# Kernel tuning notes

Hardware: AMD Instinct MI355X
Metric: run time of the kernel (lower is better)

Reference implementation:

```python
import jax, jax.numpy as jnp
import numpy as np

B, T, D = 8, 1024, 768
H, DH = 12, 64
E, K, DFF = 16, 2, 3072
EPS = 1e-5


def _ln(x, w, b):
    m = x.mean(-1, keepdims=True)
    v = ((x - m) ** 2).mean(-1, keepdims=True)
    return (x - m) * jax.lax.rsqrt(v + EPS) * w + b


def setup_inputs() -> dict:
    key = jax.random.key(0)
    ks = jax.random.split(key, 12)
    s = 0.02
    return {
        "x": jax.random.normal(ks[0], (B, T, D), jnp.float32),
        "ln1_w": jnp.ones((D,), jnp.float32),
        "ln1_b": jnp.zeros((D,), jnp.float32),
        "qkv_w": jax.random.normal(ks[1], (D, 3 * D), jnp.float32) * s,
        "qkv_b": jnp.zeros((3 * D,), jnp.float32),
        "proj_w": jax.random.normal(ks[2], (D, D), jnp.float32) * s,
        "proj_b": jnp.zeros((D,), jnp.float32),
        "ln2_w": jnp.ones((D,), jnp.float32),
        "ln2_b": jnp.zeros((D,), jnp.float32),
        "router_w": jax.random.normal(ks[3], (D, E), jnp.float32) * s,
        "w1": jax.random.normal(ks[4], (E, D, DFF), jnp.float32) * s,
        "b1": jnp.zeros((E, DFF), jnp.float32),
        "w2": jax.random.normal(ks[5], (E, DFF, D), jnp.float32) * s,
        "b2": jnp.zeros((E, D), jnp.float32),
    }


def _block(x, ln1_w, ln1_b, qkv_w, qkv_b, proj_w, proj_b,
           ln2_w, ln2_b, router_w, w1, b1, w2, b2):
    # --- attention ---
    h = _ln(x, ln1_w, ln1_b)
    qkv = h @ qkv_w + qkv_b                      # [B,T,3D]
    q, k, v = jnp.split(qkv, 3, axis=-1)
    q = q.reshape(B, T, H, DH).transpose(0, 2, 1, 3)
    k = k.reshape(B, T, H, DH).transpose(0, 2, 1, 3)
    v = v.reshape(B, T, H, DH).transpose(0, 2, 1, 3)
    scores = jnp.einsum("bhqd,bhkd->bhqk", q, k) / np.sqrt(DH)
    causal = jnp.tril(jnp.ones((T, T), bool))
    scores = jnp.where(causal, scores, -jnp.inf)
    attn = jax.nn.softmax(scores, axis=-1)
    y = jnp.einsum("bhqk,bhkd->bhqd", attn, v)
    y = y.transpose(0, 2, 1, 3).reshape(B, T, D)
    x = x + y @ proj_w + proj_b                  # residual 1

    # --- MoE FFN (dense all-experts, gated combine) ---
    z = _ln(x, ln2_w, ln2_b)                     # [B,T,D]
    probs = jax.nn.softmax(z @ router_w, axis=-1)  # [B,T,E]
    top_p, ix = jax.lax.top_k(probs, K)
    gate = (jax.nn.one_hot(ix, E, dtype=probs.dtype) * top_p[..., None]).sum(-2)  # [B,T,E]
    gate_e = jnp.moveaxis(gate, -1, 0)           # [E,B,T]

    def body(acc, ew):
        g, W1, B1, W2, B2 = ew
        out = jax.nn.gelu(z @ W1 + B1, approximate=False) @ W2 + B2
        return acc + g[..., None] * out, None

    yff, _ = jax.lax.scan(body, jnp.zeros_like(z), (gate_e, w1, b1, w2, b2))
    # MoELayer returns z + yff; Block adds x again (faithful double residual)
    return x + z + yff


def reference(x, ln1_w, ln1_b, qkv_w, qkv_b, proj_w, proj_b,
              ln2_w, ln2_b, router_w, w1, b1, w2, b2):
    return _block(x, ln1_w, ln1_b, qkv_w, qkv_b, proj_w, proj_b,
                  ln2_w, ln2_b, router_w, w1, b1, w2, b2)
```

## Files before the change

### kernel.cpp

```cpp
#include <hip/hip_runtime.h>
#include <math.h>

#define D_MODEL 768
#define T_SEQ   1024
#define B_BATCH 8
#define NTOK    8192
#define H_HEADS 12
#define DHEAD   64
#define NEXP    16
#define DFF     3072
#define NPAIR   16384
#define MAXT128 144
#define MAXT256 80

typedef unsigned short u16;
typedef unsigned int   u32;

typedef __attribute__((ext_vector_type(8))) short bf16x8;
typedef __attribute__((ext_vector_type(4))) float f32x4;
typedef __attribute__((ext_vector_type(4))) u32   u32x4;

__device__ __forceinline__ float bf2f(u16 u) { return __uint_as_float(((u32)u) << 16); }
__device__ __forceinline__ u16 f2bf(float f) {
    u32 u = __float_as_uint(f);
    return (u16)((u + 0x7FFFu + ((u >> 16) & 1u)) >> 16);
}

__device__ __forceinline__ float fast_gelu(float v) {
    float u2 = -1.5957691216f * v * (1.0f + 0.044715f * v * v);
    return v / (1.0f + __expf(u2));
}

__device__ __forceinline__ void gload16(const void* g, void* l) {
    __builtin_amdgcn_global_load_lds((const __attribute__((address_space(1))) void*)g,
                                     (__attribute__((address_space(3))) void*)l, 16, 0, 0);
}

__global__ __launch_bounds__(256) void ln_kernel(const float* __restrict__ x,
                                                 const float* __restrict__ w,
                                                 const float* __restrict__ b,
                                                 u16* __restrict__ out_bf,
                                                 float* __restrict__ out_f) {
    const int row = blockIdx.x;
    const int tid = threadIdx.x;
    const float* xr = x + (size_t)row * D_MODEL;
    float v0 = xr[tid], v1 = xr[tid + 256], v2 = xr[tid + 512];
    float s = v0 + v1 + v2;
    float s2 = v0 * v0 + v1 * v1 + v2 * v2;
#pragma unroll
    for (int o = 32; o > 0; o >>= 1) { s += __shfl_down(s, o); s2 += __shfl_down(s2, o); }
    __shared__ float red[8];
    __shared__ float stats[2];
    const int wid = tid >> 6;
    if ((tid & 63) == 0) { red[wid] = s; red[4 + wid] = s2; }
    __syncthreads();
    if (tid == 0) {
        float ts = red[0] + red[1] + red[2] + red[3];
        float ts2 = red[4] + red[5] + red[6] + red[7];
        float mean = ts * (1.0f / D_MODEL);
        float var = ts2 * (1.0f / D_MODEL) - mean * mean;
        stats[0] = mean;
        stats[1] = rsqrtf(var + 1e-5f);
    }
    __syncthreads();
    const float mean = stats[0], rstd = stats[1];
    u16* orow = out_bf + (size_t)row * D_MODEL;
    float r0 = (v0 - mean) * rstd * w[tid]       + b[tid];
    float r1 = (v1 - mean) * rstd * w[tid + 256] + b[tid + 256];
    float r2 = (v2 - mean) * rstd * w[tid + 512] + b[tid + 512];
    orow[tid] = f2bf(r0); orow[tid + 256] = f2bf(r1); orow[tid + 512] = f2bf(r2);
    if (out_f) {
        float* frow = out_f + (size_t)row * D_MODEL;
        frow[tid] = r0; frow[tid + 256] = r1; frow[tid + 512] = r2;
    }
}

__global__ __launch_bounds__(256) void transpose_cvt(const float* __restrict__ src,
                                                     u16* __restrict__ dst,
                                                     int R, int C) {
    const size_t plane = (size_t)R * C;
    src += (size_t)blockIdx.z * plane;
    dst += (size_t)blockIdx.z * plane;
    __shared__ __align__(16) u16 tile[64][72];
    const int t = threadIdx.x;
    const int r0 = blockIdx.y * 64, c0 = blockIdx.x * 64;
    {
        const int lr = t >> 2, lc = (t & 3) * 16;
        const float* sp = src + (size_t)(r0 + lr) * C + c0 + lc;
        u16 tmp[16];
#pragma unroll
        for (int j = 0; j < 4; ++j) {
            f32x4 f = *(const f32x4*)(sp + j * 4);
            tmp[j * 4 + 0] = f2bf(f[0]); tmp[j * 4 + 1] = f2bf(f[1]);
            tmp[j * 4 + 2] = f2bf(f[2]); tmp[j * 4 + 3] = f2bf(f[3]);
        }
        *(u32x4*)&tile[lr][lc]     = *(const u32x4*)&tmp[0];
        *(u32x4*)&tile[lr][lc + 8] = *(const u32x4*)&tmp[8];
    }
    __syncthreads();
    {
        const int ln = t >> 2, lk0 = (t & 3) * 16;
        u16 o[16];
#pragma unroll
        for (int j = 0; j < 16; ++j) o[j] = tile[lk0 + j][ln];
        u16* d = dst + (size_t)(c0 + ln) * R + r0 + lk0;
        *(u32x4*)&d[0] = *(const u32x4*)&o[0];
        *(u32x4*)&d[8] = *(const u32x4*)&o[8];
    }
}

template <int MODE>
__global__ __launch_bounds__(512, 2) void gemm2ph(
    const u16* __restrict__ A, const u16* __restrict__ Bt,
    const float* __restrict__ bias, void* __restrict__ Cout,
    const int* __restrict__ bucket_tok, const int* __restrict__ offsets,
    const int* __restrict__ counts, const int* __restrict__ desc_e,
    const int* __restrict__ desc_r, const int* __restrict__ tile_cnt,
    int K, int N)
{
    const u32 nwg  = gridDim.x * gridDim.y;
    const u32 orig = blockIdx.x + gridDim.x * blockIdx.y;
    const u32 flat = (nwg & 7u) ? orig : ((orig & 7u) * (nwg >> 3) + (orig >> 3));
    const int bx = (int)(flat % gridDim.x);
    const int by = (int)(flat / gridDim.x);

    int e = 0, r0 = 0, off = 0, ne = 0, row0 = 0;
    const int col0 = bx * 256;
    if constexpr (MODE >= 2) {
        if (by >= *tile_cnt) return;
        e = desc_e[by];
        r0 = desc_r[by];
        off = offsets[e];
        ne = counts[e];
    } else {
        row0 = by * 256;
    }
    if constexpr (MODE == 2) Bt += (size_t)e * D_MODEL * DFF;
    if constexpr (MODE == 3) Bt += (size_t)e * DFF * D_MODEL;

    __shared__ __align__(16) u16 As[2][256 * 64];
    __shared__ __align__(16) u16 Bs[2][256 * 64];

    const int tid = threadIdx.x;
    const int lane = tid & 63;
    const int w = tid >> 6;
    const int wm = w >> 2, wn = w & 3;
    const int fr = lane & 15, fg = lane >> 4;

    const int koff = ((((tid & 7) * 16) ^ (((tid >> 3) & 7) << 4)) >> 1);

    u32 aoff[4], boff[4];
#pragma unroll
    for (int i = 0; i < 4; ++i) {
        const int r = i * 64 + (tid >> 3);
        u32 row;
        if constexpr (MODE == 2) {
            int rb = r0 + r;
            row = (u32)bucket_tok[off + (rb < ne ? rb : 0)];
        } else if constexpr (MODE == 3) {
            int rb = r0 + r;
            row = (u32)(off + (rb < ne ? rb : (ne - 1)));
        } else {
            row = (u32)(row0 + r);
        }
        aoff[i] = row * (u32)K + (u32)koff;
        boff[i] = (u32)(col0 + r) * (u32)K + (u32)koff;
    }

    f32x4 acc[8][4] = {};
    const int nt = K >> 6;

#pragma unroll
    for (int i = 0; i < 4; ++i) gload16(A + aoff[i],  &As[0][(i * 512 + w * 64) * 8]);
#pragma unroll
    for (int i = 0; i < 4; ++i) gload16(Bt + boff[i], &Bs[0][(i * 512 + w * 64) * 8]);
    __syncthreads();

    int cur = 0;
    for (int t = 0; t < nt; ++t) {
        if (t + 1 < nt) {
            const int k0n = (t + 1) * 64;
            const int nxt = cur ^ 1;
#pragma unroll
            for (int i = 0; i < 4; ++i) gload16(A + aoff[i] + k0n,  &As[nxt][(i * 512 + w * 64) * 8]);
#pragma unroll
            for (int i = 0; i < 4; ++i) gload16(Bt + boff[i] + k0n, &Bs[nxt][(i * 512 + w * 64) * 8]);
        }
#pragma unroll
        for (int kk = 0; kk < 2; ++kk) {
            const int sw = ((kk * 64 + fg * 16) ^ ((fr & 7) << 4)) >> 1;
            bf16x8 a[8], b[4];
#pragma unroll
            for (int mi = 0; mi < 8; ++mi)
                a[mi] = *(const bf16x8*)&As[cur][(wm * 128 + mi * 16 + fr) * 64 + sw];
#pragma unroll
            for (int ni = 0; ni < 4; ++ni)
                b[ni] = *(const bf16x8*)&Bs[cur][(wn * 64 + ni * 16 + fr) * 64 + sw];
#pragma unroll
            for (int mi = 0; mi < 8; ++mi)
#pragma unroll
                for (int ni = 0; ni < 4; ++ni)
                    acc[mi][ni] = __builtin_amdgcn_mfma_f32_16x16x32_bf16(a[mi], b[ni], acc[mi][ni], 0, 0, 0);
        }
        if (t + 1 < nt) {
            __syncthreads();
            cur ^= 1;
        }
    }

    __syncthreads();
    float* slab = (float*)&As[0][0] + w * 1088;
    const int er = lane >> 2;
    const int ec = (lane & 3) * 16;
    const int colb = col0 + wn * 64 + ec;

#pragma unroll
    for (int mi = 0; mi < 8; ++mi) {
#pragma unroll
        for (int ni = 0; ni < 4; ++ni)
#pragma unroll
            for (int i = 0; i < 4; ++i)
                slab[(fg * 4 + i) * 68 + ni * 16 + fr] = acc[mi][ni][i];
        __syncthreads();
        f32x4 v[4];
#pragma unroll
        for (int q = 0; q < 4; ++q) v[q] = *(const f32x4*)&slab[er * 68 + ec + q * 4];
        const int lrow = wm * 128 + mi * 16 + er;

        if constexpr (MODE == 0) {
            u16 o[16];
#pragma unroll
            for (int q = 0; q < 4; ++q) {
                f32x4 b4 = *(const f32x4*)&bias[colb + q * 4];
#pragma unroll
                for (int j = 0; j < 4; ++j) o[q * 4 + j] = f2bf(v[q][j] + b4[j]);
            }
            u16* cp = (u16*)Cout + (size_t)(row0 + lrow) * N + colb;
            *(u32x4*)cp       = *(const u32x4*)&o[0];
            *(u32x4*)(cp + 8) = *(const u32x4*)&o[8];
        } else if constexpr (MODE == 2) {
            const int rb = r0 + lrow;
            if (rb < ne) {
                u16 o[16];
#pragma unroll
                for (int q = 0; q < 4; ++q) {
                    f32x4 b4 = *(const f32x4*)&bias[(size_t)e * DFF + colb + q * 4];
#pragma unroll
                    for (int j = 0; j < 4; ++j) o[q * 4 + j] = f2bf(fast_gelu(v[q][j] + b4[j]));
                }
                u16* cp = (u16*)Cout + (size_t)(off + rb) * N + colb;
                *(u32x4*)cp       = *(const u32x4*)&o[0];
                *(u32x4*)(cp + 8) = *(const u32x4*)&o[8];
            }
        } else {
            const int rb = r0 + lrow;
            if (rb < ne) {
                float* cp = (float*)Cout + (size_t)(off + rb) * N + colb;
#pragma unroll
                for (int q = 0; q < 4; ++q) {
                    f32x4 b4 = *(const f32x4*)&bias[(size_t)e * D_MODEL + colb + q * 4];
                    f32x4 o4;
#pragma unroll
                    for (int j = 0; j < 4; ++j) o4[j] = v[q][j] + b4[j];
                    *(f32x4*)(cp + q * 4) = o4;
                }
            }
        }
        if (mi < 7) __syncthreads();
    }
}

template <int MODE>
__global__ __launch_bounds__(512, 4) void gemm256(
    const u16* __restrict__ A, const u16* __restrict__ Bt,
    const float* __restrict__ bias, void* __restrict__ Cout,
    const float* __restrict__ resid,
    int K, int N)
{
    const u32 nwg  = gridDim.x * gridDim.y;
    const u32 orig = blockIdx.x + gridDim.x * blockIdx.y;
    const u32 flat = (nwg & 7u) ? orig : ((orig & 7u) * (nwg >> 3) + (orig >> 3));
    const int bx = (int)(flat % gridDim.x);
    const int by = (int)(flat / gridDim.x);

    const int col0 = bx * 128;
    const int row0 = by * 256;

    __shared__ __align__(16) u16 AsBs[256 * 64 + 128 * 64];
    u16* As = AsBs;
    u16* Bs = AsBs + 256 * 64;

    const int tid = threadIdx.x;
    const int lane = tid & 63;
    const int w = tid >> 6;
    const int wm = w >> 1, wn = w & 1;
    const int fr = lane & 15, fg = lane >> 4;

    const int koff = ((((tid & 7) * 16) ^ (((tid >> 3) & 7) << 4)) >> 1);

    u32 aoff[4];
#pragma unroll
    for (int i = 0; i < 4; ++i)
        aoff[i] = (u32)(row0 + i * 64 + (tid >> 3)) * (u32)K + (u32)koff;
    u32 boff[2];
#pragma unroll
    for (int i = 0; i < 2; ++i)
        boff[i] = (u32)(col0 + i * 64 + (tid >> 3)) * (u32)K + (u32)koff;

    f32x4 acc[4][4] = {};

    for (int k0 = 0; k0 < K; k0 += 64) {
        __syncthreads();
#pragma unroll
        for (int i = 0; i < 4; ++i)
            gload16(A + aoff[i] + k0, &As[(i * 512 + w * 64) * 8]);
#pragma unroll
        for (int i = 0; i < 2; ++i)
            gload16(Bt + boff[i] + k0, &Bs[(i * 512 + w * 64) * 8]);
        __syncthreads();
#pragma unroll
        for (int kk = 0; kk < 2; ++kk) {
            const int sw = ((kk * 64 + fg * 16) ^ ((fr & 7) << 4)) >> 1;
            bf16x8 a[4], b[4];
#pragma unroll
            for (int mi = 0; mi < 4; ++mi)
                a[mi] = *(const bf16x8*)&As[(wm * 64 + mi * 16 + fr) * 64 + sw];
#pragma unroll
            for (int ni = 0; ni < 4; ++ni)
                b[ni] = *(const bf16x8*)&Bs[(wn * 64 + ni * 16 + fr) * 64 + sw];
#pragma unroll
            for (int mi = 0; mi < 4; ++mi)
#pragma unroll
                for (int ni = 0; ni < 4; ++ni)
                    acc[mi][ni] = __builtin_amdgcn_mfma_f32_16x16x32_bf16(a[mi], b[ni], acc[mi][ni], 0, 0, 0);
        }
    }

    __syncthreads();
    float* slab = (float*)AsBs + w * 1088;
    const int er = lane >> 2;
    const int ec = (lane & 3) * 16;
    const int colb = col0 + wn * 64 + ec;

#pragma unroll
    for (int mi = 0; mi < 4; ++mi) {
#pragma unroll
        for (int ni = 0; ni < 4; ++ni)
#pragma unroll
            for (int i = 0; i < 4; ++i)
                slab[(fg * 4 + i) * 68 + ni * 16 + fr] = acc[mi][ni][i];
        __syncthreads();
        f32x4 v[4];
#pragma unroll
        for (int q = 0; q < 4; ++q) v[q] = *(const f32x4*)&slab[er * 68 + ec + q * 4];
        const int lrow = wm * 64 + mi * 16 + er;

        float* cp = (float*)Cout + (size_t)(row0 + lrow) * N + colb;
        const float* rp = resid + (size_t)(row0 + lrow) * N + colb;
#pragma unroll
        for (int q = 0; q < 4; ++q) {
            f32x4 b4 = *(const f32x4*)&bias[colb + q * 4];
            f32x4 r4 = *(const f32x4*)(rp + q * 4);
            f32x4 o4;
#pragma unroll
            for (int j = 0; j < 4; ++j) o4[j] = v[q][j] + b4[j] + r4[j];
            *(f32x4*)(cp + q * 4) = o4;
        }
        if (mi < 3) __syncthreads();
    }
}

template <int MODE>
__global__ __launch_bounds__(256) void gemm128f(
    const u16* __restrict__ A, const float* __restrict__ Bf,
    const float* __restrict__ bias, void* __restrict__ Cout,
    const float* __restrict__ resid,
    const int* __restrict__ bucket_tok, const int* __restrict__ offsets,
    const int* __restrict__ counts, const int* __restrict__ desc_e,
    const int* __restrict__ desc_r, const int* __restrict__ tile_cnt,
    int K, int N)
{
    int e = 0, r0 = 0, off = 0, ne = 0, row0 = 0;
    const int col0 = blockIdx.x * 128;
    if constexpr (MODE >= 2) {
        if ((int)blockIdx.y >= *tile_cnt) return;
        e = desc_e[blockIdx.y]; r0 = desc_r[blockIdx.y];
        off = offsets[e]; ne = counts[e];
    } else row0 = blockIdx.y * 128;
    if constexpr (MODE == 2) Bf += (size_t)e * D_MODEL * DFF;
    if constexpr (MODE == 3) Bf += (size_t)e * DFF * D_MODEL;

    __shared__ __align__(16) u16 AsL[128 * 32];
    __shared__ __align__(16) u16 BsL[128 * 32];

    const int tid = threadIdx.x;
    const int lane = tid & 63;
    const int w = tid >> 6;
    const int wr = (w >> 1) * 64, wc = (w & 1) * 64;
    const int fr = lane & 15, fg = lane >> 4;
    const int lrow = lane >> 2, lk = (lane & 3) * 8;

    const u16* ag[2];
#pragma unroll
    for (int i = 0; i < 2; ++i) {
        int r = i * 64 + w * 16 + lrow;
        size_t srow;
        if constexpr (MODE == 2) {
            int rb = r0 + r;
            int tok = bucket_tok[off + (rb < ne ? rb : 0)];
            srow = (size_t)tok * K;
        } else if constexpr (MODE == 3) {
            int rb = r0 + r;
            int pp = off + (rb < ne ? rb : (ne - 1));
            srow = (size_t)pp * K;
        } else srow = (size_t)(row0 + r) * K;
        ag[i] = A + srow + lk;
    }

    f32x4 acc[4][4] = {};
    for (int k0 = 0; k0 < K; k0 += 32) {
        __syncthreads();
        gload16(ag[0] + k0, &AsL[0 * 2048 + w * 512]);
        gload16(ag[1] + k0, &AsL[1 * 2048 + w * 512]);
#pragma unroll
        for (int i = 0; i < 4; ++i) {
            int s = tid + 256 * i;
            int kk = s >> 5, n4 = (s & 31) * 4;
            f32x4 f = *(const f32x4*)(Bf + (size_t)(k0 + kk) * N + col0 + n4);
            BsL[(n4 + 0) * 32 + kk] = f2bf(f[0]);
            BsL[(n4 + 1) * 32 + kk] = f2bf(f[1]);
            BsL[(n4 + 2) * 32 + kk] = f2bf(f[2]);
            BsL[(n4 + 3) * 32 + kk] = f2bf(f[3]);
        }
        __syncthreads();
        bf16x8 a[4], b[4];
#pragma unroll
        for (int mi = 0; mi < 4; ++mi)
            a[mi] = *(const bf16x8*)&AsL[(wr + mi * 16 + fr) * 32 + fg * 8];
#pragma unroll
        for (int ni = 0; ni < 4; ++ni)
            b[ni] = *(const bf16x8*)&BsL[(wc + ni * 16 + fr) * 32 + fg * 8];
#pragma unroll
        for (int mi = 0; mi < 4; ++mi)
#pragma unroll
            for (int ni = 0; ni < 4; ++ni)
                acc[mi][ni] = __builtin_amdgcn_mfma_f32_16x16x32_bf16(a[mi], b[ni], acc[mi][ni], 0, 0, 0);
    }
#pragma unroll
    for (int mi = 0; mi < 4; ++mi) {
#pragma unroll
        for (int ni = 0; ni < 4; ++ni) {
            const int lr = wr + mi * 16 + fg * 4;
            const int col = col0 + wc + ni * 16 + fr;
#pragma unroll
            for (int i = 0; i < 4; ++i) {
                float v = acc[mi][ni][i];
                if constexpr (MODE == 0) {
                    int grow = row0 + lr + i;
                    ((u16*)Cout)[(size_t)grow * N + col] = f2bf(v + bias[col]);
                } else if constexpr (MODE == 1) {
                    int grow = row0 + lr + i;
                    size_t idx = (size_t)grow * N + col;
                    ((float*)Cout)[idx] = resid[idx] + v + bias[col];
                } else if constexpr (MODE == 2) {
                    int rb = r0 + lr + i;
                    if (rb < ne) {
                        float vb = v + bias[(size_t)e * DFF + col];
                        ((u16*)Cout)[(size_t)(off + rb) * N + col] = f2bf(fast_gelu(vb));
                    }
                } else {
                    int rb = r0 + lr + i;
                    if (rb < ne) {
                        ((float*)Cout)[(size_t)(off + rb) * N + col] = v + bias[(size_t)e * D_MODEL + col];
                    }
                }
            }
        }
    }
}

__global__ __launch_bounds__(256) void attn_mfma(const u16* __restrict__ qkv,
                                                 u16* __restrict__ y) {
    const int bh = blockIdx.x;
    const int b = bh / H_HEADS, h = bh % H_HEADS;
    const int qt = gridDim.y - 1 - blockIdx.y;
    const int tid = threadIdx.x, lane = tid & 63, w = tid >> 6;
    const int fr = lane & 15, fg = lane >> 4;

    __shared__ __align__(16) u16 Ks[64][72];
    __shared__ __align__(16) u16 Vt[64][72];
    __shared__ __align__(16) u16 Ps[4][32][72];

    const int tb = b * T_SEQ + qt * 128;
    const int wrow = w * 32;

    bf16x8 aq[2][2];
#pragma unroll
    for (int rg = 0; rg < 2; ++rg) {
        const u16* qp = qkv + (size_t)(tb + wrow + rg * 16 + fr) * (3 * D_MODEL) + h * DHEAD + fg * 8;
        aq[rg][0] = *(const bf16x8*)qp;
        aq[rg][1] = *(const bf16x8*)(qp + 32);
    }
    f32x4 accO[2][4] = {};
    float m_[2][4], l_[2][4];
#pragma unroll
    for (int rg = 0; rg < 2; ++rg)
#pragma unroll
        for (int i = 0; i < 4; ++i) { m_[rg][i] = -1e30f; l_[rg][i] = 0.0f; }

    const int ktmax = 2 * qt + 1;
    for (int kt = 0; kt <= ktmax; ++kt) {
        __syncthreads();
        {
            const int krow = tid >> 2, c16 = (tid & 3) * 16;
            const u16* kp = qkv + (size_t)(b * T_SEQ + kt * 64 + krow) * (3 * D_MODEL)
                          + D_MODEL + h * DHEAD + c16;
            *(u32x4*)&Ks[krow][c16]     = *(const u32x4*)kp;
            *(u32x4*)&Ks[krow][c16 + 8] = *(const u32x4*)(kp + 8);
            const u16* vp = kp + D_MODEL;
            u16 vv[16];
            *(u32x4*)&vv[0] = *(const u32x4*)vp;
            *(u32x4*)&vv[8] = *(const u32x4*)(vp + 8);
#pragma unroll
            for (int j = 0; j < 16; ++j) Vt[c16 + j][krow] = vv[j];
        }
        __syncthreads();

        if (kt * 64 > qt * 128 + wrow + 31) continue;

#pragma unroll
        for (int rg = 0; rg < 2; ++rg) {
            f32x4 s4[4] = {};
#pragma unroll
            for (int kk = 0; kk < 2; ++kk) {
#pragma unroll
                for (int ni = 0; ni < 4; ++ni) {
                    bf16x8 bk = *(const bf16x8*)&Ks[ni * 16 + fr][kk * 32 + fg * 8];
                    s4[ni] = __builtin_amdgcn_mfma_f32_16x16x32_bf16(aq[rg][kk], bk, s4[ni], 0, 0, 0);
                }
            }
            float p[4][4];
#pragma unroll
            for (int i = 0; i < 4; ++i) {
                const int grow = qt * 128 + wrow + rg * 16 + fg * 4 + i;
                float rmax = -1e30f;
#pragma unroll
                for (int ni = 0; ni < 4; ++ni) {
                    float v = s4[ni][i] * 0.125f;
                    if (kt * 64 + ni * 16 + fr > grow) v = -1e30f;
                    p[ni][i] = v;
                    rmax = fmaxf(rmax, v);
                }
#pragma unroll
                for (int msk = 1; msk < 16; msk <<= 1) rmax = fmaxf(rmax, __shfl_xor(rmax, msk));
                const float mn = fmaxf(m_[rg][i], rmax);
                float sum = 0.0f;
#pragma unroll
                for (int ni = 0; ni < 4; ++ni) {
                    float ev = __expf(p[ni][i] - mn);
                    p[ni][i] = ev;
                    sum += ev;
                }
#pragma unroll
                for (int msk = 1; msk < 16; msk <<= 1) sum += __shfl_xor(sum, msk);
                const float sc = __expf(m_[rg][i] - mn);
                l_[rg][i] = l_[rg][i] * sc + sum;
                m_[rg][i] = mn;
#pragma unroll
                for (int ni = 0; ni < 4; ++ni) accO[rg][ni][i] *= sc;
#pragma unroll
                for (int ni = 0; ni < 4; ++ni)
                    Ps[w][rg * 16 + fg * 4 + i][ni * 16 + fr] = f2bf(p[ni][i]);
            }
        }

#pragma unroll
        for (int rg = 0; rg < 2; ++rg) {
#pragma unroll
            for (int kk = 0; kk < 2; ++kk) {
                bf16x8 ap = *(const bf16x8*)&Ps[w][rg * 16 + fr][kk * 32 + fg * 8];
#pragma unroll
                for (int ni = 0; ni < 4; ++ni) {
                    bf16x8 bv = *(const bf16x8*)&Vt[ni * 16 + fr][kk * 32 + fg * 8];
                    accO[rg][ni] = __builtin_amdgcn_mfma_f32_16x16x32_bf16(ap, bv, accO[rg][ni], 0, 0, 0);
                }
            }
        }
    }

#pragma unroll
    for (int rg = 0; rg < 2; ++rg) {
#pragma unroll
        for (int i = 0; i < 4; ++i) {
            const float inv = 1.0f / l_[rg][i];
            u16* yp = y + (size_t)(tb + wrow + rg * 16 + fg * 4 + i) * D_MODEL + h * DHEAD;
#pragma unroll
            for (int ni = 0; ni < 4; ++ni) yp[ni * 16 + fr] = f2bf(accO[rg][ni][i] * inv);
        }
    }
}

__global__ __launch_bounds__(64) void router_kernel(const float* __restrict__ z,
                                                    const float* __restrict__ rw,
                                                    float* __restrict__ gates,
                                                    int* __restrict__ eidx) {
    const int t = blockIdx.x;
    const int lane = threadIdx.x;
    const int e = lane & 15, part = lane >> 4;
    const float* zr = z + (size_t)t * D_MODEL;
    float acc = 0.0f;
    for (int d = part * 192; d < part * 192 + 192; ++d)
        acc += zr[d] * rw[d * NEXP + e];
    acc += __shfl_down(acc, 32);
    acc += __shfl_down(acc, 16);
    const float lg = acc;
    float logit[NEXP];
#pragma unroll
    for (int ee = 0; ee < NEXP; ++ee) logit[ee] = __shfl(lg, ee);
    if (lane == 0) {
        float m1 = -1e30f, m2 = -1e30f; int i1 = 0, i2 = 0;
#pragma unroll
        for (int ee = 0; ee < NEXP; ++ee) {
            float v = logit[ee];
            if (v > m1) { m2 = m1; i2 = i1; m1 = v; i1 = ee; }
            else if (v > m2) { m2 = v; i2 = ee; }
        }
        float den = 0.0f;
#pragma unroll
        for (int ee = 0; ee < NEXP; ++ee) den += __expf(logit[ee] - m1);
        const float inv = 1.0f / den;
        gates[2 * t] = inv;
        gates[2 * t + 1] = __expf(m2 - m1) * inv;
        eidx[2 * t] = i1;
        eidx[2 * t + 1] = i2;
    }
}

__global__ __launch_bounds__(256) void count_kernel(const int* __restrict__ eidx, int* counts) {
    int i = blockIdx.x * 256 + threadIdx.x;
    if (i < NPAIR) atomicAdd(&counts[eidx[i]], 1);
}

__global__ void offsets_kernel(const int* __restrict__ counts, int* offsets, int* cursor,
                               int* desc_e, int* desc_r, int* tile_cnt, int step) {
    if (threadIdx.x == 0 && blockIdx.x == 0) {
        int off = 0, nt = 0;
        for (int e = 0; e < NEXP; ++e) {
            offsets[e] = off;
            cursor[e] = off;
            int c = counts[e];
            for (int r = 0; r < c; r += step) { desc_e[nt] = e; desc_r[nt] = r; ++nt; }
            off += c;
        }
        *tile_cnt = nt;
    }
}

__global__ __launch_bounds__(256) void scatter_kernel(const int* __restrict__ eidx, int* cursor,
                                                      int* __restrict__ btok, int* __restrict__ ppos) {
    int i = blockIdx.x * 256 + threadIdx.x;
    if (i < NPAIR) {
        int pos = atomicAdd(&cursor[eidx[i]], 1);
        btok[pos] = i >> 1;
        ppos[i] = pos;
    }
}

__global__ __launch_bounds__(256) void final_kernel(const float* __restrict__ x1,
                                                    const float* __restrict__ zf,
                                                    const float* __restrict__ moe_o,
                                                    const float* __restrict__ gates,
                                                    const int* __restrict__ ppos,
                                                    float* __restrict__ out) {
    const int t = blockIdx.x;
    const int d = blockIdx.y * 256 + threadIdx.x;
    const size_t idx = (size_t)t * D_MODEL + d;
    const float g0 = gates[2 * t], g1 = gates[2 * t + 1];
    const int p0 = ppos[2 * t], p1 = ppos[2 * t + 1];
    out[idx] = x1[idx] + zf[idx] + g0 * moe_o[(size_t)p0 * D_MODEL + d]
                                 + g1 * moe_o[(size_t)p1 * D_MODEL + d];
}

extern "C" void kernel_launch(void* const* d_in, const int* in_sizes, int n_in,
                              void* d_out, int out_size, void* d_ws, size_t ws_size,
                              hipStream_t stream) {
    const float* x        = (const float*)d_in[0];
    const float* ln1_w    = (const float*)d_in[1];
    const float* ln1_b    = (const float*)d_in[2];
    const float* qkv_w    = (const float*)d_in[3];
    const float* qkv_b    = (const float*)d_in[4];
    const float* proj_w   = (const float*)d_in[5];
    const float* proj_b   = (const float*)d_in[6];
    const float* ln2_w    = (const float*)d_in[7];
    const float* ln2_b    = (const float*)d_in[8];
    const float* router_w = (const float*)d_in[9];
    const float* w1       = (const float*)d_in[10];
    const float* b1       = (const float*)d_in[11];
    const float* w2       = (const float*)d_in[12];
    const float* b2       = (const float*)d_in[13];
    float* out = (float*)d_out;

    char* ws = (char*)d_ws;
    size_t off = 0;
    auto alloc = [&](size_t bytes) -> void* {
        void* p = ws + off;
        off += (bytes + 255) & ~(size_t)255;
        return p;
    };
    u16*  h_bf   = (u16*)alloc((size_t)NTOK * D_MODEL * 2);
    u16*  qkv_bf = (u16*)alloc((size_t)NTOK * 3 * D_MODEL * 2);
    u16*  y_bf   = h_bf;
    float* x1    = (float*)alloc((size_t)NTOK * D_MODEL * 4);
    u16*  z_bf   = (u16*)alloc((size_t)NTOK * D_MODEL * 2);
    float* z_f   = (float*)alloc((size_t)NTOK * D_MODEL * 4);
    u16*  act    = (u16*)alloc((size_t)NPAIR * DFF * 2);
    float* moe_o = (float*)alloc((size_t)NPAIR * D_MODEL * 4);
    float* gates = (float*)alloc((size_t)NTOK * 2 * 4);
    int*  eidx   = (int*)alloc((size_t)NTOK * 2 * 4);
    int*  ppos   = (int*)alloc((size_t)NTOK * 2 * 4);
    int*  btok   = (int*)alloc((size_t)NPAIR * 4);
    int*  counts = (int*)alloc(NEXP * 4);
    int*  offs   = (int*)alloc(NEXP * 4);
    int*  cursor = (int*)alloc(NEXP * 4);
    int*  desc_e = (int*)alloc(MAXT128 * 4);
    int*  desc_r = (int*)alloc(MAXT128 * 4);
    int*  tcnt   = (int*)alloc(4);
    u16* qkvT  = (u16*)alloc((size_t)(3 * D_MODEL) * D_MODEL * 2);
    u16* projT = (u16*)alloc((size_t)D_MODEL * D_MODEL * 2);
    u16* w1t   = (u16*)alloc((size_t)NEXP * DFF * D_MODEL * 2);
    u16* w2t   = (u16*)alloc((size_t)NEXP * D_MODEL * DFF * 2);
    const bool useT = (off <= ws_size);
    (void)in_sizes; (void)n_in; (void)out_size;

    hipMemsetAsync(counts, 0, NEXP * 4, stream);

    if (useT) {
        transpose_cvt<<<dim3(3 * D_MODEL / 64, D_MODEL / 64, 1), 256, 0, stream>>>(qkv_w, qkvT, D_MODEL, 3 * D_MODEL);
        transpose_cvt<<<dim3(D_MODEL / 64, D_MODEL / 64, 1), 256, 0, stream>>>(proj_w, projT, D_MODEL, D_MODEL);
        transpose_cvt<<<dim3(DFF / 64, D_MODEL / 64, NEXP), 256, 0, stream>>>(w1, w1t, D_MODEL, DFF);
        transpose_cvt<<<dim3(D_MODEL / 64, DFF / 64, NEXP), 256, 0, stream>>>(w2, w2t, DFF, D_MODEL);
    }

    ln_kernel<<<NTOK, 256, 0, stream>>>(x, ln1_w, ln1_b, h_bf, nullptr);
    if (useT)
        gemm2ph<0><<<dim3(9, 32), 512, 0, stream>>>(h_bf, qkvT, qkv_b, qkv_bf,
            nullptr, nullptr, nullptr, nullptr, nullptr, nullptr, D_MODEL, 3 * D_MODEL);
    else
        gemm128f<0><<<dim3(18, 64), 256, 0, stream>>>(h_bf, qkv_w, qkv_b, qkv_bf, nullptr,
            nullptr, nullptr, nullptr, nullptr, nullptr, nullptr, D_MODEL, 3 * D_MODEL);

    attn_mfma<<<dim3(B_BATCH * H_HEADS, T_SEQ / 128), 256, 0, stream>>>(qkv_bf, y_bf);

    if (useT)
        gemm256<1><<<dim3(6, 32), 512, 0, stream>>>(y_bf, projT, proj_b, x1, x,
            D_MODEL, D_MODEL);
    else
        gemm128f<1><<<dim3(6, 64), 256, 0, stream>>>(y_bf, proj_w, proj_b, x1, x,
            nullptr, nullptr, nullptr, nullptr, nullptr, nullptr, D_MODEL, D_MODEL);

    ln_kernel<<<NTOK, 256, 0, stream>>>(x1, ln2_w, ln2_b, z_bf, z_f);
    router_kernel<<<NTOK, 64, 0, stream>>>(z_f, router_w, gates, eidx);
    count_kernel<<<NPAIR / 256, 256, 0, stream>>>(eidx, counts);
    offsets_kernel<<<1, 64, 0, stream>>>(counts, offs, cursor, desc_e, desc_r, tcnt,
                                         useT ? 256 : 128);
    scatter_kernel<<<NPAIR / 256, 256, 0, stream>>>(eidx, cursor, btok, ppos);

    if (useT) {
        gemm2ph<2><<<dim3(DFF / 256, MAXT256), 512, 0, stream>>>(z_bf, w1t, b1, act,
            btok, offs, counts, desc_e, desc_r, tcnt, D_MODEL, DFF);
        gemm2ph<3><<<dim3(D_MODEL / 256, MAXT256), 512, 0, stream>>>(act, w2t, b2, moe_o,
            btok, offs, counts, desc_e, desc_r, tcnt, DFF, D_MODEL);
    } else {
        gemm128f<2><<<dim3(DFF / 128, MAXT128), 256, 0, stream>>>(z_bf, w1, b1, act, nullptr,
            btok, offs, counts, desc_e, desc_r, tcnt, D_MODEL, DFF);
        gemm128f<3><<<dim3(D_MODEL / 128, MAXT128), 256, 0, stream>>>(act, w2, b2, moe_o, nullptr,
            btok, offs, counts, desc_e, desc_r, tcnt, DFF, D_MODEL);
    }

    final_kernel<<<dim3(NTOK, 3), 256, 0, stream>>>(x1, z_f, moe_o, gates, ppos, out);
}
```

Before: 659.1 us.

## Fold softmax scale into QKV GEMM, skip masks, lazy rescale, vectorize final combine

The QKV GEMM epilogue now multiplies the Q columns by 1/sqrt(64), so attention no longer scales every score. Attention skips per-element causal masking on fully unmasked key tiles and rescales the output accumulator only when the running max increases. It also raises wave priority around the MFMA sections. The final combine kernel now uses float4 loads and stores with one 192-thread block per token. Together these trim ALU work inside attention and make the final pass cheaper, at the cost of extra branching and a Q stored in bf16 after scaling.

Result: no change. 665.7 us (+1.0%).

```diff
diff --git a/kernel.cpp b/kernel.cpp
--- a/kernel.cpp
+++ b/kernel.cpp
@@ -228,12 +228,13 @@
         const int lrow = wm * 128 + mi * 16 + er;
 
         if constexpr (MODE == 0) {
+            const float qs = (colb < D_MODEL) ? 0.125f : 1.0f;
             u16 o[16];
 #pragma unroll
             for (int q = 0; q < 4; ++q) {
                 f32x4 b4 = *(const f32x4*)&bias[colb + q * 4];
 #pragma unroll
-                for (int j = 0; j < 4; ++j) o[q * 4 + j] = f2bf(v[q][j] + b4[j]);
+                for (int j = 0; j < 4; ++j) o[q * 4 + j] = f2bf((v[q][j] + b4[j]) * qs);
             }
             u16* cp = (u16*)Cout + (size_t)(row0 + lrow) * N + colb;
             *(u32x4*)cp       = *(const u32x4*)&o[0];
@@ -457,7 +458,8 @@
                 float v = acc[mi][ni][i];
                 if constexpr (MODE == 0) {
                     int grow = row0 + lr + i;
-                    ((u16*)Cout)[(size_t)grow * N + col] = f2bf(v + bias[col]);
+                    const float qs = (col < D_MODEL) ? 0.125f : 1.0f;
+                    ((u16*)Cout)[(size_t)grow * N + col] = f2bf((v + bias[col]) * qs);
                 } else if constexpr (MODE == 1) {
                     int grow = row0 + lr + i;
                     size_t idx = (size_t)grow * N + col;
@@ -527,10 +529,12 @@
         __syncthreads();
 
         if (kt * 64 > qt * 128 + wrow + 31) continue;
+        const bool nomask = (kt * 64 + 63) <= (qt * 128 + wrow);
 
 #pragma unroll
         for (int rg = 0; rg < 2; ++rg) {
             f32x4 s4[4] = {};
+            __builtin_amdgcn_s_setprio(1);
 #pragma unroll
             for (int kk = 0; kk < 2; ++kk) {
 #pragma unroll
@@ -539,21 +543,38 @@
                     s4[ni] = __builtin_amdgcn_mfma_f32_16x16x32_bf16(aq[rg][kk], bk, s4[ni], 0, 0, 0);
                 }
             }
+            __builtin_amdgcn_s_setprio(0);
             float p[4][4];
 #pragma unroll
             for (int i = 0; i < 4; ++i) {
-                const int grow = qt * 128 + wrow + rg * 16 + fg * 4 + i;
                 float rmax = -1e30f;
-#pragma unroll
-                for (int ni = 0; ni < 4; ++ni) {
-                    float v = s4[ni][i] * 0.125f;
-                    if (kt * 64 + ni * 16 + fr > grow) v = -1e30f;
-                    p[ni][i] = v;
-                    rmax = fmaxf(rmax, v);
+                if (nomask) {
+#pragma unroll
+                    for (int ni = 0; ni < 4; ++ni) {
+                        p[ni][i] = s4[ni][i];
+                        rmax = fmaxf(rmax, p[ni][i]);
+                    }
+                } else {
+                    const int grow = qt * 128 + wrow + rg * 16 + fg * 4 + i;
+#pragma unroll
+                    for (int ni = 0; ni < 4; ++ni) {
+                        float v = s4[ni][i];
+                        if (kt * 64 + ni * 16 + fr > grow) v = -1e30f;
+                        p[ni][i] = v;
+                        rmax = fmaxf(rmax, v);
+                    }
                 }
 #pragma unroll
                 for (int msk = 1; msk < 16; msk <<= 1) rmax = fmaxf(rmax, __shfl_xor(rmax, msk));
-                const float mn = fmaxf(m_[rg][i], rmax);
+                float mn = m_[rg][i];
+                if (rmax > mn) {
+                    const float sc = __expf(mn - rmax);
+                    l_[rg][i] *= sc;
+#pragma unroll
+                    for (int ni = 0; ni < 4; ++ni) accO[rg][ni][i] *= sc;
+                    mn = rmax;
+                    m_[rg][i] = rmax;
+                }
                 float sum = 0.0f;
 #pragma unroll
                 for (int ni = 0; ni < 4; ++ni) {
@@ -563,17 +584,14 @@
                 }
 #pragma unroll
                 for (int msk = 1; msk < 16; msk <<= 1) sum += __shfl_xor(sum, msk);
-                const float sc = __expf(m_[rg][i] - mn);
-                l_[rg][i] = l_[rg][i] * sc + sum;
-                m_[rg][i] = mn;
-#pragma unroll
-                for (int ni = 0; ni < 4; ++ni) accO[rg][ni][i] *= sc;
+                l_[rg][i] += sum;
 #pragma unroll
                 for (int ni = 0; ni < 4; ++ni)
                     Ps[w][rg * 16 + fg * 4 + i][ni * 16 + fr] = f2bf(p[ni][i]);
             }
         }
 
+        __builtin_amdgcn_s_setprio(1);
 #pragma unroll
         for (int rg = 0; rg < 2; ++rg) {
 #pragma unroll
@@ -586,6 +604,7 @@
                 }
             }
         }
+        __builtin_amdgcn_s_setprio(0);
     }
 
 #pragma unroll
@@ -666,19 +685,25 @@
     }
 }
 
-__global__ __launch_bounds__(256) void final_kernel(const float* __restrict__ x1,
+__global__ __launch_bounds__(192) void final_kernel(const float* __restrict__ x1,
                                                     const float* __restrict__ zf,
                                                     const float* __restrict__ moe_o,
                                                     const float* __restrict__ gates,
                                                     const int* __restrict__ ppos,
                                                     float* __restrict__ out) {
     const int t = blockIdx.x;
-    const int d = blockIdx.y * 256 + threadIdx.x;
-    const size_t idx = (size_t)t * D_MODEL + d;
+    const int d4 = threadIdx.x * 4;
+    const size_t idx = (size_t)t * D_MODEL + d4;
     const float g0 = gates[2 * t], g1 = gates[2 * t + 1];
     const int p0 = ppos[2 * t], p1 = ppos[2 * t + 1];
-    out[idx] = x1[idx] + zf[idx] + g0 * moe_o[(size_t)p0 * D_MODEL + d]
-                                 + g1 * moe_o[(size_t)p1 * D_MODEL + d];
+    f32x4 a = *(const f32x4*)&x1[idx];
+    f32x4 zz = *(const f32x4*)&zf[idx];
+    f32x4 m0 = *(const f32x4*)&moe_o[(size_t)p0 * D_MODEL + d4];
+    f32x4 m1 = *(const f32x4*)&moe_o[(size_t)p1 * D_MODEL + d4];
+    f32x4 o;
+#pragma unroll
+    for (int j = 0; j < 4; ++j) o[j] = a[j] + zz[j] + g0 * m0[j] + g1 * m1[j];
+    *(f32x4*)&out[idx] = o;
 }
 
 extern "C" void kernel_launch(void* const* d_in, const int* in_sizes, int n_in,
@@ -777,5 +802,5 @@
             btok, offs, counts, desc_e, desc_r, tcnt, DFF, D_MODEL);
     }
 
-    final_kernel<<<dim3(NTOK, 3), 256, 0, stream>>>(x1, z_f, moe_o, gates, ppos, out);
-}
+    final_kernel<<<NTOK, 192, 0, stream>>>(x1, z_f, moe_o, gates, ppos, out);
+}
```

## Fuse MoE combine into down-proj epilogue via atomics; widen attention key tiles to 128

Applied to the files above, without the earlier changes.

LN2 now also writes x1+z straight into the output. The second expert GEMM scatter-adds the gated result into that output with float atomics, so the separate combine kernel and its moe_o round trip are gone. Separately, attention now processes 128-key tiles per iteration, applying the causal mask only on the diagonal tile, which halves the loop trips and the barriers. The atomics add contention and make the summation order non-deterministic, and the larger shared-memory tiles may lower occupancy.

Measured after the change: 1.339 ms. +103.2%, slower.

```diff
diff --git a/kernel.cpp b/kernel.cpp
--- a/kernel.cpp
+++ b/kernel.cpp
@@ -40,7 +40,8 @@
                                                  const float* __restrict__ w,
                                                  const float* __restrict__ b,
                                                  u16* __restrict__ out_bf,
-                                                 float* __restrict__ out_f) {
+                                                 float* __restrict__ out_f,
+                                                 float* __restrict__ base_out) {
     const int row = blockIdx.x;
     const int tid = threadIdx.x;
     const float* xr = x + (size_t)row * D_MODEL;
@@ -73,6 +74,10 @@
         float* frow = out_f + (size_t)row * D_MODEL;
         frow[tid] = r0; frow[tid + 256] = r1; frow[tid + 512] = r2;
     }
+    if (base_out) {
+        float* brow = base_out + (size_t)row * D_MODEL;
+        brow[tid] = v0 + r0; brow[tid + 256] = v1 + r1; brow[tid + 512] = v2 + r2;
+    }
 }
 
 __global__ __launch_bounds__(256) void transpose_cvt(const float* __restrict__ src,
@@ -113,7 +118,8 @@
 __global__ __launch_bounds__(512, 2) void gemm2ph(
     const u16* __restrict__ A, const u16* __restrict__ Bt,
     const float* __restrict__ bias, void* __restrict__ Cout,
-    const int* __restrict__ bucket_tok, const int* __restrict__ offsets,
+    const int* __restrict__ bucket_tok, const float* __restrict__ bgate,
+    const int* __restrict__ offsets,
     const int* __restrict__ counts, const int* __restrict__ desc_e,
     const int* __restrict__ desc_r, const int* __restrict__ tile_cnt,
     int K, int N)
@@ -255,14 +261,15 @@
         } else {
             const int rb = r0 + lrow;
             if (rb < ne) {
-                float* cp = (float*)Cout + (size_t)(off + rb) * N + colb;
+                const int tok = bucket_tok[off + rb];
+                const float g = bgate[off + rb];
+                float* cp = (float*)Cout + (size_t)tok * N + colb;
 #pragma unroll
                 for (int q = 0; q < 4; ++q) {
                     f32x4 b4 = *(const f32x4*)&bias[(size_t)e * D_MODEL + colb + q * 4];
-                    f32x4 o4;
-#pragma unroll
-                    for (int j = 0; j < 4; ++j) o4[j] = v[q][j] + b4[j];
-                    *(f32x4*)(cp + q * 4) = o4;
+#pragma unroll
+                    for (int j = 0; j < 4; ++j)
+                        atomicAdd(cp + q * 4 + j, g * (v[q][j] + b4[j]));
                 }
             }
         }
@@ -487,9 +494,9 @@
     const int tid = threadIdx.x, lane = tid & 63, w = tid >> 6;
     const int fr = lane & 15, fg = lane >> 4;
 
-    __shared__ __align__(16) u16 Ks[64][72];
-    __shared__ __align__(16) u16 Vt[64][72];
-    __shared__ __align__(16) u16 Ps[4][32][72];
+    __shared__ __align__(16) u16 Ks[128][72];
+    __shared__ __align__(16) u16 Vt[64][136];
+    __shared__ __align__(16) u16 Ps[4][32][136];
 
     const int tb = b * T_SEQ + qt * 128;
     const int wrow = w * 32;
@@ -508,55 +515,67 @@
 #pragma unroll
         for (int i = 0; i < 4; ++i) { m_[rg][i] = -1e30f; l_[rg][i] = 0.0f; }
 
-    const int ktmax = 2 * qt + 1;
-    for (int kt = 0; kt <= ktmax; ++kt) {
+    for (int kt = 0; kt <= qt; ++kt) {
         __syncthreads();
         {
-            const int krow = tid >> 2, c16 = (tid & 3) * 16;
-            const u16* kp = qkv + (size_t)(b * T_SEQ + kt * 64 + krow) * (3 * D_MODEL)
-                          + D_MODEL + h * DHEAD + c16;
-            *(u32x4*)&Ks[krow][c16]     = *(const u32x4*)kp;
-            *(u32x4*)&Ks[krow][c16 + 8] = *(const u32x4*)(kp + 8);
-            const u16* vp = kp + D_MODEL;
-            u16 vv[16];
-            *(u32x4*)&vv[0] = *(const u32x4*)vp;
-            *(u32x4*)&vv[8] = *(const u32x4*)(vp + 8);
-#pragma unroll
-            for (int j = 0; j < 16; ++j) Vt[c16 + j][krow] = vv[j];
+#pragma unroll
+            for (int it = 0; it < 2; ++it) {
+                const int krow = (tid >> 2) + it * 64;
+                const int c16 = (tid & 3) * 16;
+                const u16* kp = qkv + (size_t)(b * T_SEQ + kt * 128 + krow) * (3 * D_MODEL)
+                              + D_MODEL + h * DHEAD + c16;
+                *(u32x4*)&Ks[krow][c16]     = *(const u32x4*)kp;
+                *(u32x4*)&Ks[krow][c16 + 8] = *(const u32x4*)(kp + 8);
+                const u16* vp = kp + D_MODEL;
+                u16 vv[16];
+                *(u32x4*)&vv[0] = *(const u32x4*)vp;
+                *(u32x4*)&vv[8] = *(const u32x4*)(vp + 8);
+#pragma unroll
+                for (int j = 0; j < 16; ++j) Vt[c16 + j][krow] = vv[j];
+            }
         }
         __syncthreads();
 
-        if (kt * 64 > qt * 128 + wrow + 31) continue;
+        const bool diag = (kt == qt);
 
 #pragma unroll
         for (int rg = 0; rg < 2; ++rg) {
-            f32x4 s4[4] = {};
+            f32x4 s4[8] = {};
 #pragma unroll
             for (int kk = 0; kk < 2; ++kk) {
 #pragma unroll
-                for (int ni = 0; ni < 4; ++ni) {
+                for (int ni = 0; ni < 8; ++ni) {
                     bf16x8 bk = *(const bf16x8*)&Ks[ni * 16 + fr][kk * 32 + fg * 8];
                     s4[ni] = __builtin_amdgcn_mfma_f32_16x16x32_bf16(aq[rg][kk], bk, s4[ni], 0, 0, 0);
                 }
             }
-            float p[4][4];
+            float p[8][4];
 #pragma unroll
             for (int i = 0; i < 4; ++i) {
                 const int grow = qt * 128 + wrow + rg * 16 + fg * 4 + i;
                 float rmax = -1e30f;
-#pragma unroll
-                for (int ni = 0; ni < 4; ++ni) {
-                    float v = s4[ni][i] * 0.125f;
-                    if (kt * 64 + ni * 16 + fr > grow) v = -1e30f;
-                    p[ni][i] = v;
-                    rmax = fmaxf(rmax, v);
+                if (!diag) {
+#pragma unroll
+                    for (int ni = 0; ni < 8; ++ni) {
+                        float v = s4[ni][i] * 0.125f;
+                        p[ni][i] = v;
+                        rmax = fmaxf(rmax, v);
+                    }
+                } else {
+#pragma unroll
+                    for (int ni = 0; ni < 8; ++ni) {
+                        float v = s4[ni][i] * 0.125f;
+                        if (kt * 128 + ni * 16 + fr > grow) v = -1e30f;
+                        p[ni][i] = v;
+                        rmax = fmaxf(rmax, v);
+                    }
                 }
 #pragma unroll
                 for (int msk = 1; msk < 16; msk <<= 1) rmax = fmaxf(rmax, __shfl_xor(rmax, msk));
                 const float mn = fmaxf(m_[rg][i], rmax);
                 float sum = 0.0f;
 #pragma unroll
-                for (int ni = 0; ni < 4; ++ni) {
+                for (int ni = 0; ni < 8; ++ni) {
                     float ev = __expf(p[ni][i] - mn);
                     p[ni][i] = ev;
                     sum += ev;
@@ -569,7 +588,7 @@
 #pragma unroll
                 for (int ni = 0; ni < 4; ++ni) accO[rg][ni][i] *= sc;
 #pragma unroll
-                for (int ni = 0; ni < 4; ++ni)
+                for (int ni = 0; ni < 8; ++ni)
                     Ps[w][rg * 16 + fg * 4 + i][ni * 16 + fr] = f2bf(p[ni][i]);
             }
         }
@@ -577,7 +596,7 @@
 #pragma unroll
         for (int rg = 0; rg < 2; ++rg) {
 #pragma unroll
-            for (int kk = 0; kk < 2; ++kk) {
+            for (int kk = 0; kk < 4; ++kk) {
                 bf16x8 ap = *(const bf16x8*)&Ps[w][rg * 16 + fr][kk * 32 + fg * 8];
 #pragma unroll
                 for (int ni = 0; ni < 4; ++ni) {
@@ -657,11 +676,15 @@
 }
 
 __global__ __launch_bounds__(256) void scatter_kernel(const int* __restrict__ eidx, int* cursor,
-                                                      int* __restrict__ btok, int* __restrict__ ppos) {
+                                                      const float* __restrict__ gates,
+                                                      int* __restrict__ btok,
+                                                      float* __restrict__ bgate,
+                                                      int* __restrict__ ppos) {
     int i = blockIdx.x * 256 + threadIdx.x;
     if (i < NPAIR) {
         int pos = atomicAdd(&cursor[eidx[i]], 1);
         btok[pos] = i >> 1;
+        bgate[pos] = gates[i];
         ppos[i] = pos;
     }
 }
@@ -719,6 +742,7 @@
     int*  eidx   = (int*)alloc((size_t)NTOK * 2 * 4);
     int*  ppos   = (int*)alloc((size_t)NTOK * 2 * 4);
     int*  btok   = (int*)alloc((size_t)NPAIR * 4);
+    float* bgate = (float*)alloc((size_t)NPAIR * 4);
     int*  counts = (int*)alloc(NEXP * 4);
     int*  offs   = (int*)alloc(NEXP * 4);
     int*  cursor = (int*)alloc(NEXP * 4);
@@ -741,10 +765,10 @@
         transpose_cvt<<<dim3(D_MODEL / 64, DFF / 64, NEXP), 256, 0, stream>>>(w2, w2t, DFF, D_MODEL);
     }
 
-    ln_kernel<<<NTOK, 256, 0, stream>>>(x, ln1_w, ln1_b, h_bf, nullptr);
+    ln_kernel<<<NTOK, 256, 0, stream>>>(x, ln1_w, ln1_b, h_bf, nullptr, nullptr);
     if (useT)
         gemm2ph<0><<<dim3(9, 32), 512, 0, stream>>>(h_bf, qkvT, qkv_b, qkv_bf,
-            nullptr, nullptr, nullptr, nullptr, nullptr, nullptr, D_MODEL, 3 * D_MODEL);
+            nullptr, nullptr, nullptr, nullptr, nullptr, nullptr, nullptr, D_MODEL, 3 * D_MODEL);
     else
         gemm128f<0><<<dim3(18, 64), 256, 0, stream>>>(h_bf, qkv_w, qkv_b, qkv_bf, nullptr,
             nullptr, nullptr, nullptr, nullptr, nullptr, nullptr, D_MODEL, 3 * D_MODEL);
@@ -758,24 +782,23 @@
         gemm128f<1><<<dim3(6, 64), 256, 0, stream>>>(y_bf, proj_w, proj_b, x1, x,
             nullptr, nullptr, nullptr, nullptr, nullptr, nullptr, D_MODEL, D_MODEL);
 
-    ln_kernel<<<NTOK, 256, 0, stream>>>(x1, ln2_w, ln2_b, z_bf, z_f);
+    ln_kernel<<<NTOK, 256, 0, stream>>>(x1, ln2_w, ln2_b, z_bf, z_f, useT ? out : nullptr);
     router_kernel<<<NTOK, 64, 0, stream>>>(z_f, router_w, gates, eidx);
     count_kernel<<<NPAIR / 256, 256, 0, stream>>>(eidx, counts);
     offsets_kernel<<<1, 64, 0, stream>>>(counts, offs, cursor, desc_e, desc_r, tcnt,
                                          useT ? 256 : 128);
-    scatter_kernel<<<NPAIR / 256, 256, 0, stream>>>(eidx, cursor, btok, ppos);
+    scatter_kernel<<<NPAIR / 256, 256, 0, stream>>>(eidx, cursor, gates, btok, bgate, ppos);
 
     if (useT) {
         gemm2ph<2><<<dim3(DFF / 256, MAXT256), 512, 0, stream>>>(z_bf, w1t, b1, act,
-            btok, offs, counts, desc_e, desc_r, tcnt, D_MODEL, DFF);
-        gemm2ph<3><<<dim3(D_MODEL / 256, MAXT256), 512, 0, stream>>>(act, w2t, b2, moe_o,
-            btok, offs, counts, desc_e, desc_r, tcnt, DFF, D_MODEL);
+            btok, nullptr, offs, counts, desc_e, desc_r, tcnt, D_MODEL, DFF);
+        gemm2ph<3><<<dim3(D_MODEL / 256, MAXT256), 512, 0, stream>>>(act, w2t, b2, out,
+            btok, bgate, offs, counts, desc_e, desc_r, tcnt, DFF, D_MODEL);
     } else {
         gemm128f<2><<<dim3(DFF / 128, MAXT128), 256, 0, stream>>>(z_bf, w1, b1, act, nullptr,
             btok, offs, counts, desc_e, desc_r, tcnt, D_MODEL, DFF);
         gemm128f<3><<<dim3(D_MODEL / 128, MAXT128), 256, 0, stream>>>(act, w2, b2, moe_o, nullptr,
             btok, offs, counts, desc_e, desc_r, tcnt, DFF, D_MODEL);
-    }
-
-    final_kernel<<<dim3(NTOK, 3), 256, 0, stream>>>(x1, z_f, moe_o, gates, ppos, out);
-}
+        final_kernel<<<dim3(NTOK, 3), 256, 0, stream>>>(x1, z_f, moe_o, gates, ppos, out);
+    }
+}
```
